# Kernel optimization log

Measured on AMD Instinct MI355X. Metric: run time of the kernel, lower is better.

## Reference

```python
import jax, jax.numpy as jnp
import numpy as np

D_MODEL = 2048
NUM_HEADS = 16
D_HEAD = D_MODEL // NUM_HEADS
MAX_SEQ_LEN = 2048
THETA = 10000.0


def setup_inputs() -> dict:
    key = jax.random.key(0)
    kx, kq, kk, kv, ko = jax.random.split(key, 5)
    std = float(np.sqrt(2.0 / (D_MODEL + D_MODEL)))
    def tn(k):
        # truncated normal in [-3std, 3std] scaled by std
        return std * jax.random.truncated_normal(k, -3.0, 3.0, (D_MODEL, D_MODEL), jnp.float32)
    return {
        "x": jax.random.normal(kx, (2, MAX_SEQ_LEN, D_MODEL), jnp.float32),
        "w_q": tn(kq),
        "w_k": tn(kk),
        "w_v": tn(kv),
        "w_o": tn(ko),
    }


def _rope(x):
    # x: [B, H, S, Dh], default positions = arange(S)
    S = x.shape[-2]
    pos = jnp.arange(S, dtype=jnp.float32)
    inv_freq = 1.0 / (THETA ** (jnp.arange(0, D_HEAD, 2, dtype=jnp.float32) / D_HEAD))
    ang = pos[:, None] * inv_freq[None, :]           # [S, Dh/2]
    cos = jnp.cos(ang).astype(x.dtype)
    sin = jnp.sin(ang).astype(x.dtype)
    x_even = x[..., 0::2]
    x_odd = x[..., 1::2]
    out_even = x_even * cos - x_odd * sin
    out_odd = x_even * sin + x_odd * cos
    # interleave even/odd back
    return jnp.stack([out_even, out_odd], axis=-1).reshape(x.shape)


def reference(x, w_q, w_k, w_v, w_o):
    B, S, _ = x.shape
    def split_heads(t):
        return t.reshape(B, S, NUM_HEADS, D_HEAD).transpose(0, 2, 1, 3)  # [B,H,S,Dh]
    q = split_heads(x @ w_q.T)
    k = split_heads(x @ w_k.T)
    v = split_heads(x @ w_v.T)
    q = _rope(q)
    k = _rope(k)
    scores = jnp.einsum('bhqd,bhkd->bhqk', q, k) / jnp.sqrt(jnp.asarray(D_HEAD, x.dtype))
    causal = jnp.tril(jnp.ones((S, S), dtype=bool))
    scores = jnp.where(causal, scores, jnp.finfo(scores.dtype).min)
    attn = jax.nn.softmax(scores, axis=-1)
    out = jnp.einsum('bhqk,bhkd->bhqd', attn, v)     # [B,H,S,Dh]
    out = out.transpose(0, 2, 1, 3).reshape(B, S, D_MODEL)
    return out @ w_o.T
```

## Files before the change

### kernel.cpp

```cpp
#include <hip/hip_runtime.h>
#include <hip/hip_bf16.h>

typedef __bf16 bf16;
typedef __bf16 bf16x8 __attribute__((ext_vector_type(8)));
typedef __bf16 bf16x4 __attribute__((ext_vector_type(4)));
typedef float f32x4 __attribute__((ext_vector_type(4)));

#define MFMA_BF16(a, b, c) __builtin_amdgcn_mfma_f32_16x16x32_bf16(a, b, c, 0, 0, 0)

constexpr int D_MODEL = 2048;
constexpr int NUM_HEADS = 16;
constexpr int D_HEAD = 128;
constexpr int SEQ = 2048;
constexpr int BATCH = 2;
constexpr int M_TOTAL = BATCH * SEQ;

__device__ __forceinline__ void gld_lds16(const bf16* g, bf16* l) {
  __builtin_amdgcn_global_load_lds((const __attribute__((address_space(1))) void*)g,
                                   (__attribute__((address_space(3))) void*)l, 16, 0, 0);
}

__global__ __launch_bounds__(256) void cvt_all(const float* __restrict__ x,
                                               const float* __restrict__ wq,
                                               const float* __restrict__ wk,
                                               const float* __restrict__ wv,
                                               const float* __restrict__ wo,
                                               bf16* __restrict__ dst) {
  const long i = (long)blockIdx.x * 256 + threadIdx.x;
  const float* src;
  long off;
  if (i < 2097152) {
    src = x; off = i;
  } else {
    const long j = i - 2097152;
    const int w = (int)(j >> 20);
    off = j & 1048575;
    src = (w == 0) ? wq : (w == 1) ? wk : (w == 2) ? wv : wo;
  }
  float4 v = reinterpret_cast<const float4*>(src)[off];
  bf16x4 o;
  o[0] = (bf16)v.x; o[1] = (bf16)v.y; o[2] = (bf16)v.z; o[3] = (bf16)v.w;
  reinterpret_cast<bf16x4*>(dst)[i] = o;
}

enum { EP_F32 = 0, EP_QKV = 1 };

template <int EPI>
__global__ __launch_bounds__(256) void gemm_bt(const bf16* __restrict__ A,
                                               const bf16* __restrict__ B,
                                               void* __restrict__ C0,
                                               void* __restrict__ C1,
                                               void* __restrict__ C2,
                                               int M, int N, int K) {
  __shared__ __align__(16) bf16 As[128 * 32];
  __shared__ __align__(16) bf16 Bs[128 * 32];
  const int tid = threadIdx.x;
  const int lane = tid & 63;
  const int wave = tid >> 6;
  const int lane15 = lane & 15;
  const int quad = lane >> 4;
  const int m0 = blockIdx.y * 128;
  const int n0 = blockIdx.x * 128;
  const int wm = (wave >> 1) * 64;
  const int wn = (wave & 1) * 64;

  const int srow = wave * 16 + (lane >> 2);
  const int skc = ((lane & 3) ^ ((lane >> 3) & 3)) * 8;
  const bf16* gA = A + (long)(m0 + srow) * K + skc;
  const bf16* gB = B + (long)(n0 + srow) * K + skc;
  const long roff = (long)64 * K;
  bf16* lA0 = As + wave * 512;
  bf16* lA1 = As + 2048 + wave * 512;
  bf16* lB0 = Bs + wave * 512;
  bf16* lB1 = Bs + 2048 + wave * 512;
  const int swq = (quad ^ ((lane15 >> 1) & 3)) * 8;

  f32x4 acc[4][4];
#pragma unroll
  for (int i = 0; i < 4; ++i)
#pragma unroll
    for (int j = 0; j < 4; ++j) acc[i][j] = (f32x4){0.f, 0.f, 0.f, 0.f};

  for (int k0 = 0; k0 < K; k0 += 32) {
    __syncthreads();
    gld_lds16(gA + k0, lA0);
    gld_lds16(gA + roff + k0, lA1);
    gld_lds16(gB + k0, lB0);
    gld_lds16(gB + roff + k0, lB1);
    __syncthreads();

    bf16x8 af[4], bfr[4];
#pragma unroll
    for (int i = 0; i < 4; ++i)
      af[i] = *reinterpret_cast<const bf16x8*>(&As[(wm + i * 16 + lane15) * 32 + swq]);
#pragma unroll
    for (int j = 0; j < 4; ++j)
      bfr[j] = *reinterpret_cast<const bf16x8*>(&Bs[(wn + j * 16 + lane15) * 32 + swq]);
#pragma unroll
    for (int i = 0; i < 4; ++i)
#pragma unroll
      for (int j = 0; j < 4; ++j)
        acc[i][j] = MFMA_BF16(af[i], bfr[j], acc[i][j]);
  }

  if (EPI == EP_F32) {
#pragma unroll
    for (int i = 0; i < 4; ++i)
#pragma unroll
      for (int j = 0; j < 4; ++j)
#pragma unroll
        for (int r = 0; r < 4; ++r) {
          const int m = m0 + wm + i * 16 + quad * 4 + r;
          const int n = n0 + wn + j * 16 + lane15;
          reinterpret_cast<float*>(C0)[(long)m * N + n] = acc[i][j][r];
        }
  } else {
    const int mat = n0 >> 11;
    bf16* dst = (mat == 0) ? (bf16*)C0 : (mat == 1) ? (bf16*)C1 : (bf16*)C2;
    const int nb = n0 & 2047;
    if (mat < 2) {
#pragma unroll
      for (int i = 0; i < 4; ++i)
#pragma unroll
        for (int j = 0; j < 4; ++j)
#pragma unroll
          for (int r = 0; r < 4; ++r) {
            const int m = m0 + wm + i * 16 + quad * 4 + r;
            const int nl = nb + wn + j * 16 + lane15;
            const int b = m >> 11;
            const int s = m & (SEQ - 1);
            const int h = nl >> 7;
            const int d = nl & (D_HEAD - 1);
            float v = acc[i][j][r];
            float other = __shfl_xor(v, 1);
            float fr = exp2f((float)(d & ~1) * -0.103810253f);
            float ang = (float)s * fr;
            float sn = __sinf(ang);
            float cs = __cosf(ang);
            float outv = (lane15 & 1) ? (v * cs + other * sn) : (v * cs - other * sn);
            dst[(((long)(b * NUM_HEADS + h)) * SEQ + s) * D_HEAD + d] = (bf16)outv;
          }
    } else {
      const int h = nb >> 7;
#pragma unroll
      for (int i = 0; i < 4; ++i)
#pragma unroll
        for (int j = 0; j < 4; ++j) {
          bf16x4 pk;
#pragma unroll
          for (int r = 0; r < 4; ++r) pk[r] = (bf16)acc[i][j][r];
          const int m = m0 + wm + i * 16 + quad * 4;
          const int b = m >> 11;
          const int s = m & (SEQ - 1);
          const int d = wn + j * 16 + lane15;
          *reinterpret_cast<bf16x4*>(
              &dst[(((long)(b * NUM_HEADS + h)) * D_HEAD + d) * SEQ + s]) = pk;
        }
    }
  }
}

__global__ __launch_bounds__(256) void flash_attn(const bf16* __restrict__ Q,
                                                  const bf16* __restrict__ K,
                                                  const bf16* __restrict__ Vt,
                                                  bf16* __restrict__ O) {
  __shared__ __align__(16) bf16 Kl[2][64 * 128];
  __shared__ __align__(16) bf16 Vl[2][128 * 64];
  __shared__ __align__(16) bf16 P[4 * 16 * 72];
  const int tid = threadIdx.x;
  const int lane = tid & 63;
  const int wave = tid >> 6;
  const int lane15 = lane & 15;
  const int quad = lane >> 4;
  const int idx = blockIdx.x >> 3;
  const int bh = (blockIdx.x & 7) * 4 + (idx & 3);
  const int qcg = 31 - (idx >> 2);
  const int q0 = qcg * 64 + wave * 16;
  const long base = (long)bh * SEQ * D_HEAD;
  const bf16* qp = Q + base;
  const bf16* kp = K + base;
  const bf16* vp = Vt + base;
  bf16* Pw = &P[wave * 16 * 72];
  constexpr float scale = 0.08838834764831845f;
  constexpr float SMAX = 30.0f;

  int ksrc[4], vsrc[4];
  const int kdst = wave * 512;
#pragma unroll
  for (int i = 0; i < 4; ++i) {
    const int c = i * 256 + tid;
    const int krow = c >> 4;
    ksrc[i] = krow * D_HEAD + (((c & 15) ^ (krow & 15)) * 8);
    const int vd = c >> 3;
    vsrc[i] = vd * SEQ + (((c & 7) ^ (vd & 7)) * 8);
  }

  bf16x8 bq[4];
#pragma unroll
  for (int kk = 0; kk < 4; ++kk)
    bq[kk] = *reinterpret_cast<const bf16x8*>(qp + (long)(q0 + lane15) * D_HEAD + kk * 32 + quad * 8);

  f32x4 o_acc[8];
#pragma unroll
  for (int dj = 0; dj < 8; ++dj) o_acc[dj] = (f32x4){0.f, 0.f, 0.f, 0.f};
  float l_part = 0.f;
  const int qcol = q0 + lane15;

  const int nkt = qcg + 1;

#pragma unroll
  for (int i = 0; i < 4; ++i) gld_lds16(kp + ksrc[i], &Kl[0][i * 2048 + kdst]);
#pragma unroll
  for (int i = 0; i < 4; ++i) gld_lds16(vp + vsrc[i], &Vl[0][i * 2048 + kdst]);
  __syncthreads();

  for (int kt = 0; kt < nkt; ++kt) {
    const int k0 = kt * 64;
    const int buf = kt & 1;

    if (kt + 1 < nkt) {
      const int nk0 = k0 + 64;
#pragma unroll
      for (int i = 0; i < 4; ++i) gld_lds16(kp + nk0 * D_HEAD + ksrc[i], &Kl[buf ^ 1][i * 2048 + kdst]);
#pragma unroll
      for (int i = 0; i < 4; ++i) gld_lds16(vp + nk0 + vsrc[i], &Vl[buf ^ 1][i * 2048 + kdst]);
    }

    f32x4 sc[4];
#pragma unroll
    for (int j = 0; j < 4; ++j) sc[j] = (f32x4){0.f, 0.f, 0.f, 0.f};
#pragma unroll
    for (int j = 0; j < 4; ++j) {
#pragma unroll
      for (int kk = 0; kk < 4; ++kk) {
        bf16x8 ak = *reinterpret_cast<const bf16x8*>(
            &Kl[buf][(j * 16 + lane15) * D_HEAD + (((kk * 4 + quad) ^ lane15) * 8)]);
        sc[j] = MFMA_BF16(ak, bq[kk], sc[j]);
      }
    }

#pragma unroll
    for (int j = 0; j < 4; ++j) {
      bf16x4 pk;
#pragma unroll
      for (int r = 0; r < 4; ++r) {
        const int kpos = k0 + j * 16 + quad * 4 + r;
        float p = (kpos <= qcol) ? __expf(sc[j][r] * scale - SMAX) : 0.f;
        l_part += p;
        pk[r] = (bf16)p;
      }
      *reinterpret_cast<bf16x4*>(&Pw[lane15 * 72 + j * 16 + quad * 4]) = pk;
    }

#pragma unroll
    for (int kc = 0; kc < 2; ++kc) {
      bf16x8 ap = *reinterpret_cast<const bf16x8*>(&Pw[lane15 * 72 + kc * 32 + quad * 8]);
#pragma unroll
      for (int dj = 0; dj < 8; ++dj) {
        bf16x8 bv = *reinterpret_cast<const bf16x8*>(
            &Vl[buf][(dj * 16 + lane15) * 64 + (((kc * 4 + quad) ^ (lane15 & 7)) * 8)]);
        o_acc[dj] = MFMA_BF16(ap, bv, o_acc[dj]);
      }
    }

    __syncthreads();
  }

  float lsum = l_part;
  lsum += __shfl_xor(lsum, 16);
  lsum += __shfl_xor(lsum, 32);

  const int b = bh >> 4;
  const int h = bh & 15;
#pragma unroll
  for (int r = 0; r < 4; ++r) {
    const float lr = __shfl(lsum, quad * 4 + r);
    const float inv_l = 1.0f / lr;
    const int qrow = q0 + quad * 4 + r;
#pragma unroll
    for (int dj = 0; dj < 8; ++dj)
      O[((long)b * SEQ + qrow) * D_MODEL + h * D_HEAD + dj * 16 + lane15] =
          (bf16)(o_acc[dj][r] * inv_l);
  }
}

extern "C" void kernel_launch(void* const* d_in, const int* in_sizes, int n_in,
                              void* d_out, int out_size, void* d_ws, size_t ws_size,
                              hipStream_t stream) {
  const float* x = (const float*)d_in[0];
  const float* wq = (const float*)d_in[1];
  const float* wk = (const float*)d_in[2];
  const float* wv = (const float*)d_in[3];
  const float* wo = (const float*)d_in[4];
  float* out = (float*)d_out;

  char* ws = (char*)d_ws;
  size_t off = 0;
  bf16* x_bf = (bf16*)(ws + off);  off += (size_t)M_TOTAL * D_MODEL * 2;
  bf16* wq_bf = (bf16*)(ws + off); off += (size_t)D_MODEL * D_MODEL * 2;
  bf16* wk_bf = (bf16*)(ws + off); off += (size_t)D_MODEL * D_MODEL * 2;
  bf16* wv_bf = (bf16*)(ws + off); off += (size_t)D_MODEL * D_MODEL * 2;
  bf16* wo_bf = (bf16*)(ws + off); off += (size_t)D_MODEL * D_MODEL * 2;
  bf16* q_r = (bf16*)(ws + off);   off += (size_t)M_TOTAL * D_MODEL * 2;
  bf16* k_r = (bf16*)(ws + off);   off += (size_t)M_TOTAL * D_MODEL * 2;
  bf16* vt_r = (bf16*)(ws + off);  off += (size_t)M_TOTAL * D_MODEL * 2;
  bf16* a_o = (bf16*)(ws + off);   off += (size_t)M_TOTAL * D_MODEL * 2;

  dim3 blk(256);
  cvt_all<<<24576, blk, 0, stream>>>(x, wq, wk, wv, wo, x_bf);

  gemm_bt<EP_QKV><<<dim3(3 * D_MODEL / 128, M_TOTAL / 128), blk, 0, stream>>>(
      x_bf, wq_bf, q_r, k_r, vt_r, M_TOTAL, 3 * D_MODEL, D_MODEL);

  flash_attn<<<dim3(1024), blk, 0, stream>>>(q_r, k_r, vt_r, a_o);

  gemm_bt<EP_F32><<<dim3(D_MODEL / 128, M_TOTAL / 128), blk, 0, stream>>>(
      a_o, wo_bf, out, nullptr, nullptr, M_TOTAL, D_MODEL, D_MODEL);
}
```

Baseline: 387.0 us.

## Rewrite GEMM with 256x128 tiles, triple-buffered LDS pipeline and XCD block swizzle

The bf16 GEMM now runs 512 threads per block on a 256x128 output tile with a K step of 64, and keeps three LDS stages filled via direct global-to-LDS loads issued two iterations ahead. Each iteration is split into two MFMA phases that overlap with the next stage's loads, using explicit waitcnt, barriers and setprio. Block indices are remapped so consecutive tiles land on the same XCD to improve L2 reuse. The aim is to hide global memory latency and cut the per-32-K double sync, at the cost of much higher LDS use (about 144KB) and register pressure.

```diff
diff --git a/kernel.cpp b/kernel.cpp
--- a/kernel.cpp
+++ b/kernel.cpp
@@ -46,34 +46,42 @@
 enum { EP_F32 = 0, EP_QKV = 1 };
 
 template <int EPI>
-__global__ __launch_bounds__(256) void gemm_bt(const bf16* __restrict__ A,
-                                               const bf16* __restrict__ B,
-                                               void* __restrict__ C0,
-                                               void* __restrict__ C1,
-                                               void* __restrict__ C2,
-                                               int M, int N, int K) {
-  __shared__ __align__(16) bf16 As[128 * 32];
-  __shared__ __align__(16) bf16 Bs[128 * 32];
+__global__ __launch_bounds__(512, 2) void gemm_bt(const bf16* __restrict__ A,
+                                                  const bf16* __restrict__ B,
+                                                  void* __restrict__ C0,
+                                                  void* __restrict__ C1,
+                                                  void* __restrict__ C2,
+                                                  int M, int N, int K) {
+  __shared__ __align__(16) bf16 As[3][256 * 64];
+  __shared__ __align__(16) bf16 Bs[3][128 * 64];
   const int tid = threadIdx.x;
   const int lane = tid & 63;
   const int wave = tid >> 6;
   const int lane15 = lane & 15;
   const int quad = lane >> 4;
-  const int m0 = blockIdx.y * 128;
-  const int n0 = blockIdx.x * 128;
+
+  const int nwg = gridDim.x;
+  const int cpx = nwg >> 3;
+  const int swz = (blockIdx.x & 7) * cpx + (blockIdx.x >> 3);
+  const int NBX = N >> 7;
+  const int m0 = (swz / NBX) * 256;
+  const int n0 = (swz % NBX) * 128;
+
   const int wm = (wave >> 1) * 64;
   const int wn = (wave & 1) * 64;
 
-  const int srow = wave * 16 + (lane >> 2);
-  const int skc = ((lane & 3) ^ ((lane >> 3) & 3)) * 8;
-  const bf16* gA = A + (long)(m0 + srow) * K + skc;
-  const bf16* gB = B + (long)(n0 + srow) * K + skc;
-  const long roff = (long)64 * K;
-  bf16* lA0 = As + wave * 512;
-  bf16* lA1 = As + 2048 + wave * 512;
-  bf16* lB0 = Bs + wave * 512;
-  bf16* lB1 = Bs + 2048 + wave * 512;
-  const int swq = (quad ^ ((lane15 >> 1) & 3)) * 8;
+  const int trow = tid >> 3;
+  const int tchk = (tid & 7) ^ (trow & 7);
+  const int wvoff = wave * 512;
+  long a_off[4], b_off[2];
+#pragma unroll
+  for (int i = 0; i < 4; ++i) a_off[i] = (long)(m0 + i * 64 + trow) * K + tchk * 8;
+#pragma unroll
+  for (int i = 0; i < 2; ++i) b_off[i] = (long)(n0 + i * 64 + trow) * K + tchk * 8;
+
+  const int r7 = lane15 & 7;
+  const int ca0 = (quad ^ r7) * 8;
+  const int ca1 = ((quad + 4) ^ r7) * 8;
 
   f32x4 acc[4][4];
 #pragma unroll
@@ -81,26 +89,91 @@
 #pragma unroll
     for (int j = 0; j < 4; ++j) acc[i][j] = (f32x4){0.f, 0.f, 0.f, 0.f};
 
-  for (int k0 = 0; k0 < K; k0 += 32) {
-    __syncthreads();
-    gld_lds16(gA + k0, lA0);
-    gld_lds16(gA + roff + k0, lA1);
-    gld_lds16(gB + k0, lB0);
-    gld_lds16(gB + roff + k0, lB1);
-    __syncthreads();
-
-    bf16x8 af[4], bfr[4];
-#pragma unroll
-    for (int i = 0; i < 4; ++i)
-      af[i] = *reinterpret_cast<const bf16x8*>(&As[(wm + i * 16 + lane15) * 32 + swq]);
-#pragma unroll
-    for (int j = 0; j < 4; ++j)
-      bfr[j] = *reinterpret_cast<const bf16x8*>(&Bs[(wn + j * 16 + lane15) * 32 + swq]);
-#pragma unroll
-    for (int i = 0; i < 4; ++i)
-#pragma unroll
-      for (int j = 0; j < 4; ++j)
-        acc[i][j] = MFMA_BF16(af[i], bfr[j], acc[i][j]);
+  const int NT = K >> 6;
+
+#pragma unroll
+  for (int i = 0; i < 4; ++i) gld_lds16(A + a_off[i], &As[0][i * 4096 + wvoff]);
+#pragma unroll
+  for (int i = 0; i < 2; ++i) gld_lds16(B + b_off[i], &Bs[0][i * 4096 + wvoff]);
+#pragma unroll
+  for (int i = 0; i < 4; ++i) gld_lds16(A + a_off[i] + 64, &As[1][i * 4096 + wvoff]);
+#pragma unroll
+  for (int i = 0; i < 2; ++i) gld_lds16(B + b_off[i] + 64, &Bs[1][i * 4096 + wvoff]);
+  asm volatile("s_waitcnt vmcnt(6)" ::: "memory");
+  __builtin_amdgcn_s_barrier();
+  __builtin_amdgcn_sched_barrier(0);
+
+  int bcur = 0, bstg = 2;
+  for (int t = 0; t < NT; ++t) {
+    const bf16* Ab = As[bcur];
+    const bf16* Bb = Bs[bcur];
+    const long kst = (long)(t + 2) * 64;
+    const bool st = (t + 2 < NT);
+
+    bf16x8 bfrg[4][2], afrg[2][2];
+#pragma unroll
+    for (int j = 0; j < 4; ++j) {
+      const int rb = (wn + j * 16 + lane15) * 64;
+      bfrg[j][0] = *reinterpret_cast<const bf16x8*>(&Bb[rb + ca0]);
+      bfrg[j][1] = *reinterpret_cast<const bf16x8*>(&Bb[rb + ca1]);
+    }
+#pragma unroll
+    for (int i = 0; i < 2; ++i) {
+      const int ra = (wm + i * 16 + lane15) * 64;
+      afrg[i][0] = *reinterpret_cast<const bf16x8*>(&Ab[ra + ca0]);
+      afrg[i][1] = *reinterpret_cast<const bf16x8*>(&Ab[ra + ca1]);
+    }
+    if (st) {
+#pragma unroll
+      for (int i = 0; i < 3; ++i)
+        gld_lds16(A + a_off[i] + kst, &As[bstg][i * 4096 + wvoff]);
+    }
+    __builtin_amdgcn_s_barrier();
+    __builtin_amdgcn_sched_barrier(0);
+    __builtin_amdgcn_s_setprio(1);
+#pragma unroll
+    for (int i = 0; i < 2; ++i)
+#pragma unroll
+      for (int j = 0; j < 4; ++j) {
+        acc[i][j] = MFMA_BF16(afrg[i][0], bfrg[j][0], acc[i][j]);
+        acc[i][j] = MFMA_BF16(afrg[i][1], bfrg[j][1], acc[i][j]);
+      }
+    __builtin_amdgcn_s_setprio(0);
+
+#pragma unroll
+    for (int i = 0; i < 2; ++i) {
+      const int ra = (wm + (i + 2) * 16 + lane15) * 64;
+      afrg[i][0] = *reinterpret_cast<const bf16x8*>(&Ab[ra + ca0]);
+      afrg[i][1] = *reinterpret_cast<const bf16x8*>(&Ab[ra + ca1]);
+    }
+    if (st) {
+      gld_lds16(A + a_off[3] + kst, &As[bstg][3 * 4096 + wvoff]);
+      gld_lds16(B + b_off[0] + kst, &Bs[bstg][0 * 4096 + wvoff]);
+      gld_lds16(B + b_off[1] + kst, &Bs[bstg][1 * 4096 + wvoff]);
+    }
+    __builtin_amdgcn_s_barrier();
+    __builtin_amdgcn_sched_barrier(0);
+    __builtin_amdgcn_s_setprio(1);
+#pragma unroll
+    for (int i = 0; i < 2; ++i)
+#pragma unroll
+      for (int j = 0; j < 4; ++j) {
+        acc[i + 2][j] = MFMA_BF16(afrg[i][0], bfrg[j][0], acc[i + 2][j]);
+        acc[i + 2][j] = MFMA_BF16(afrg[i][1], bfrg[j][1], acc[i + 2][j]);
+      }
+    __builtin_amdgcn_s_setprio(0);
+
+    if (st) {
+      asm volatile("s_waitcnt vmcnt(6)" ::: "memory");
+      __builtin_amdgcn_s_barrier();
+      __builtin_amdgcn_sched_barrier(0);
+    } else if (t == NT - 2) {
+      asm volatile("s_waitcnt vmcnt(0)" ::: "memory");
+      __builtin_amdgcn_s_barrier();
+      __builtin_amdgcn_sched_barrier(0);
+    }
+    bstg = bcur;
+    bcur = (bcur == 2) ? 0 : bcur + 1;
   }
 
   if (EPI == EP_F32) {
@@ -306,14 +379,13 @@
   bf16* vt_r = (bf16*)(ws + off);  off += (size_t)M_TOTAL * D_MODEL * 2;
   bf16* a_o = (bf16*)(ws + off);   off += (size_t)M_TOTAL * D_MODEL * 2;
 
-  dim3 blk(256);
-  cvt_all<<<24576, blk, 0, stream>>>(x, wq, wk, wv, wo, x_bf);
-
-  gemm_bt<EP_QKV><<<dim3(3 * D_MODEL / 128, M_TOTAL / 128), blk, 0, stream>>>(
+  cvt_all<<<24576, dim3(256), 0, stream>>>(x, wq, wk, wv, wo, x_bf);
+
+  gemm_bt<EP_QKV><<<dim3((M_TOTAL / 256) * (3 * D_MODEL / 128)), dim3(512), 0, stream>>>(
       x_bf, wq_bf, q_r, k_r, vt_r, M_TOTAL, 3 * D_MODEL, D_MODEL);
 
-  flash_attn<<<dim3(1024), blk, 0, stream>>>(q_r, k_r, vt_r, a_o);
-
-  gemm_bt<EP_F32><<<dim3(D_MODEL / 128, M_TOTAL / 128), blk, 0, stream>>>(
+  flash_attn<<<dim3(1024), dim3(256), 0, stream>>>(q_r, k_r, vt_r, a_o);
+
+  gemm_bt<EP_F32><<<dim3((M_TOTAL / 256) * (D_MODEL / 128)), dim3(512), 0, stream>>>(
       a_o, wo_bf, out, nullptr, nullptr, M_TOTAL, D_MODEL, D_MODEL);
 }
```

After: 351.1 us. 1.1x faster.
